# Kernel optimization log

Hardware: AMD Instinct MI355X
Metric: run time of the kernel (lower is better)

## Reference

```python
import jax, jax.numpy as jnp
import numpy as np

B, N, D = 4, 10000, 64
C, E = 2, 160000  # adj channels, edges per (graph, channel)
EPS = 1e-10


def setup_inputs() -> dict:
    key = jax.random.key(0)
    k1, k2, k3 = jax.random.split(key, 3)
    inputs = jax.random.normal(k1, (B, N, D), dtype=jnp.float32)
    edge_idx = jax.random.randint(k2, (B, C, E, 2), 0, N, dtype=jnp.int32)
    weight_a = 0.1 * jax.random.normal(k3, (C, 2 * D, 1), dtype=jnp.float32)
    return {"inputs": inputs, "edge_idx": edge_idx, "weight_a": weight_a}


def _gat_channel(x, idx, wa):
    # x: [N, D], idx: [E, 2] (col 0 = scatter/dst node, col 1 = gather/src node), wa: [2D, 1]
    n = x.shape[0]
    a1 = x[idx[:, 1]]                      # [E, D]
    a2 = x[idx[:, 0]]                      # [E, D]
    score = jnp.concatenate([a1, a2], axis=1) @ wa   # [E, 1]
    e = jnp.exp(jax.nn.leaky_relu(score, negative_slope=0.2))  # [E, 1]
    denom = jax.ops.segment_sum(e, idx[:, 0], num_segments=n)  # [N, 1]  (ii @ e)
    denom_e = denom[idx[:, 1]]             # [E, 1]  (faithful to original: gather by idx[:,1])
    alpha = e / (denom_e + EPS)            # [E, 1]
    r = jax.ops.segment_sum(alpha * a1, idx[:, 0], num_segments=n)  # [N, D]
    return jax.nn.sigmoid(r)


def _gat_graph(x, idx_all, weight_a):
    # x: [N, D], idx_all: [C, E, 2], weight_a: [C, 2D, 1]
    per_ch = jax.vmap(_gat_channel, in_axes=(None, 0, 0))(x, idx_all, weight_a)  # [C, N, D]
    return per_ch.sum(axis=0)


def reference(inputs, edge_idx, weight_a):
    # inputs: [B, N, D], edge_idx: [B, C, E, 2], weight_a: [C, 2D, 1]
    return jax.vmap(_gat_graph, in_axes=(0, 0, None))(inputs, edge_idx, weight_a)
```

## Files before the change

kernel.cpp:

```cpp
#include <hip/hip_runtime.h>

#define B_ 4
#define N_ 10000
#define D_ 64
#define C_ 2
#define E_ 160000
#define BC_ (B_ * C_)
#define SH2_ 7
#define NB2_ 128
#define G2_ 79
#define CAPF_ 2560
#define NBLK_ 125
#define EPT_ 5
#define EPB_ (256 * EPT_)
#define YBLK_ (BC_ * 40)
#define EPS_ 1e-10f

__global__ void gat_yb(const float* __restrict__ x, const float* __restrict__ wa,
                       float* __restrict__ y1, float* __restrict__ y0,
                       const int* __restrict__ eidx, int* __restrict__ gcount,
                       unsigned int* __restrict__ bpack) {
    int tid = threadIdx.x;
    if (blockIdx.x < YBLK_) {
        int bc = blockIdx.x & 7;
        int n  = (blockIdx.x >> 3) * 256 + tid;
        if (n >= N_) return;
        int b = bc / C_, c = bc % C_;
        const float4* xr = (const float4*)(x + ((size_t)b * N_ + n) * D_);
        const float4* w1 = (const float4*)(wa + (size_t)c * 2 * D_);
        const float4* w0 = w1 + D_ / 4;
        float a = 0.f, bb = 0.f;
#pragma unroll
        for (int i = 0; i < D_ / 4; ++i) {
            float4 xv = xr[i];
            float4 u = w1[i], v = w0[i];
            a  += xv.x * u.x + xv.y * u.y + xv.z * u.z + xv.w * u.w;
            bb += xv.x * v.x + xv.y * v.y + xv.z * v.z + xv.w * v.w;
        }
        y1[bc * N_ + n] = a;
        y0[bc * N_ + n] = bb;
        return;
    }
    int bid = blockIdx.x - YBLK_;
    int bc  = bid & 7;
    int blk = bid >> 3;
    const int2* ep = (const int2*)eidx + (size_t)bc * E_ + (size_t)blk * EPB_;
    __shared__ int sd[128];
    __shared__ int excl[G2_], cur[G2_], gbase[G2_];
    __shared__ unsigned int stage[EPB_];
    if (tid < 128) sd[tid] = 0;
    __syncthreads();
    unsigned int pk[EPT_];
    int gg[EPT_];
#pragma unroll
    for (int k = 0; k < EPT_; ++k) {
        int2 v = ep[k * 256 + tid];
        int g  = v.x >> SH2_;
        gg[k]  = g;
        pk[k]  = ((unsigned int)g << 21) |
                 ((unsigned int)(v.x & (NB2_ - 1)) << 14) |
                 (unsigned int)v.y;
        atomicAdd(&sd[g], 1);
    }
    __syncthreads();
    int cnt = (tid < 128) ? sd[tid] : 0;
    for (int off = 1; off < 128; off <<= 1) {
        int t = (tid < 128 && tid >= off) ? sd[tid - off] : 0;
        __syncthreads();
        if (tid < 128) sd[tid] += t;
        __syncthreads();
    }
    if (tid < G2_) {
        int ex = sd[tid] - cnt;
        excl[tid]  = ex;
        cur[tid]   = ex;
        gbase[tid] = atomicAdd(&gcount[bc * G2_ + tid], cnt);
    }
    __syncthreads();
#pragma unroll
    for (int k = 0; k < EPT_; ++k) {
        int slot = atomicAdd(&cur[gg[k]], 1);
        stage[slot] = pk[k];
    }
    __syncthreads();
#pragma unroll
    for (int k = 0; k < EPT_; ++k) {
        int idx = k * 256 + tid;
        unsigned int p = stage[idx];
        int g     = p >> 21;
        int local = idx - excl[g];
        bpack[((size_t)bc * G2_ + g) * CAPF_ + gbase[g] + local] =
            (((p >> 14) & 127u) << 16) | (p & 16383u);
    }
}

__global__ void gat_fine(const unsigned int* __restrict__ bpack,
                         const int* __restrict__ gcount,
                         const float* __restrict__ y1, const float* __restrict__ y0,
                         unsigned short* __restrict__ csr_i1,
                         int* __restrict__ rs_s, int* __restrict__ rs_e,
                         float2* __restrict__ yrd) {
    int bc = blockIdx.x & 7;
    int g  = blockIdx.x >> 3;
    int K  = gcount[bc * G2_ + g];
    int R  = (bc * G2_ + g) * CAPF_;
    const unsigned int* bp = bpack + R;
    const float* y1p = y1 + bc * N_;
    int tid = threadIdx.x;

    __shared__ int   cnt[NB2_], excl[NB2_], cur[NB2_], sd[NB2_];
    __shared__ float y0l[NB2_], den[NB2_];
    __shared__ unsigned short li1[CAPF_];

    int node = g * NB2_ + tid;
    if (tid < NB2_) {
        cnt[tid] = 0;
        den[tid] = 0.f;
        y0l[tid] = (node < N_) ? y0[bc * N_ + node] : 0.f;
    }
    __syncthreads();

    for (int j = tid; j < K; j += 256) {
        unsigned int p = bp[j];
        int ln = p >> 16;
        int i1 = p & 0xffff;
        float sc = y1p[i1] + y0l[ln];
        float ev = __expf(sc > 0.f ? sc : 0.2f * sc);
        atomicAdd(&cnt[ln], 1);
        atomicAdd(&den[ln], ev);
    }
    __syncthreads();

    int v = 0;
    if (tid < NB2_) { v = cnt[tid]; sd[tid] = v; }
    __syncthreads();
    for (int off = 1; off < NB2_; off <<= 1) {
        int t = (tid < NB2_ && tid >= off) ? sd[tid - off] : 0;
        __syncthreads();
        if (tid < NB2_) sd[tid] += t;
        __syncthreads();
    }
    if (tid < NB2_) {
        int ex = sd[tid] - v;
        excl[tid] = ex;
        cur[tid]  = ex;
        if (node < N_) {
            rs_s[bc * N_ + node] = R + ex;
            rs_e[bc * N_ + node] = R + ex + v;
            yrd[bc * N_ + node]  = make_float2(y1p[node], 1.f / (den[tid] + EPS_));
        }
    }
    __syncthreads();

    for (int j = tid; j < K; j += 256) {
        unsigned int p = bp[j];
        int slot = atomicAdd(&cur[p >> 16], 1);
        li1[slot] = (unsigned short)(p & 0xffff);
    }
    __syncthreads();

    for (int j = tid; j < K; j += 256)
        csr_i1[R + j] = li1[j];
}

__global__ void gat_acc(const float* __restrict__ x, const int* __restrict__ rs_s,
                        const int* __restrict__ rs_e,
                        const unsigned short* __restrict__ csr_i1,
                        const float2* __restrict__ yrd, const float* __restrict__ y0,
                        float* __restrict__ out) {
    int lane = threadIdx.x & 63;
    int w    = threadIdx.x >> 6;
    int b    = blockIdx.x & 3;
    int nn   = blockIdx.x >> 2;
    int n    = nn * 2 + (w >> 1);
    int c    = w & 1;
    int bc = b * C_ + c;
    const float* xb = x + (size_t)b * N_ * D_ + lane;
    const float2* yrdp = yrd + bc * N_;
    int s = rs_s[bc * N_ + n], t = rs_e[bc * N_ + n];
    float y0n = y0[bc * N_ + n];
    __shared__ float2 meta[4][64];
    float acc = 0.f;
    for (int base = s; base < t; base += 64) {
        int m = t - base; if (m > 64) m = 64;
        int a = 0; float wgt = 0.f;
        if (lane < m) {
            a = csr_i1[base + lane];
            float2 yr = yrdp[a];
            float sc = yr.x + y0n;
            wgt = __expf(sc > 0.f ? sc : 0.2f * sc) * yr.y;
        }
        meta[w][lane] = make_float2(__int_as_float(a), wgt);
        int mp = (m + 7) & ~7;
        for (int j = 0; j < mp; j += 8) {
            float2 m0 = meta[w][j],     m1 = meta[w][j + 1];
            float2 m2 = meta[w][j + 2], m3 = meta[w][j + 3];
            float2 m4 = meta[w][j + 4], m5 = meta[w][j + 5];
            float2 m6 = meta[w][j + 6], m7 = meta[w][j + 7];
            float x0 = xb[__float_as_int(m0.x) * D_], x1 = xb[__float_as_int(m1.x) * D_];
            float x2 = xb[__float_as_int(m2.x) * D_], x3 = xb[__float_as_int(m3.x) * D_];
            float x4 = xb[__float_as_int(m4.x) * D_], x5 = xb[__float_as_int(m5.x) * D_];
            float x6 = xb[__float_as_int(m6.x) * D_], x7 = xb[__float_as_int(m7.x) * D_];
            acc += m0.y * x0;
            acc += m1.y * x1;
            acc += m2.y * x2;
            acc += m3.y * x3;
            acc += m4.y * x4;
            acc += m5.y * x5;
            acc += m6.y * x6;
            acc += m7.y * x7;
        }
    }
    float sg = 1.f / (1.f + __expf(-acc));
    __shared__ float sh[2][64];
    if (c == 1) sh[w >> 1][lane] = sg;
    __syncthreads();
    if (c == 0) out[((size_t)b * N_ + n) * D_ + lane] = sg + sh[w >> 1][lane];
}

extern "C" void kernel_launch(void* const* d_in, const int* in_sizes, int n_in,
                              void* d_out, int out_size, void* d_ws, size_t ws_size,
                              hipStream_t stream) {
    const float* x    = (const float*)d_in[0];
    const int*   eidx = (const int*)d_in[1];
    const float* wa   = (const float*)d_in[2];
    float* out = (float*)d_out;

    int*    gcount = (int*)d_ws;
    float*  y1     = (float*)d_ws + 1024;
    float*  y0     = y1 + BC_ * N_;
    float2* yrd    = (float2*)(y0 + BC_ * N_);
    int*    rs_s   = (int*)(yrd + BC_ * N_);
    int*    rs_e   = rs_s + BC_ * N_;
    unsigned int* bpack = (unsigned int*)(rs_e + BC_ * N_);
    unsigned short* csr_i1 = (unsigned short*)(bpack + (size_t)BC_ * G2_ * CAPF_);

    hipMemsetAsync(gcount, 0, BC_ * G2_ * sizeof(int), stream);

    gat_yb  <<<YBLK_ + BC_ * NBLK_, 256, 0, stream>>>(x, wa, y1, y0, eidx, gcount, bpack);
    gat_fine<<<BC_ * G2_,           256, 0, stream>>>(bpack, gcount, y1, y0,
                                                      csr_i1, rs_s, rs_e, yrd);
    gat_acc <<<B_ * N_ / 2,         256, 0, stream>>>(x, rs_s, rs_e, csr_i1, yrd, y0, out);
}
```

Measured before the change: 129.3 us.

## Process four consecutive destination nodes per wavefront in gather-accumulate kernel

Each wavefront in the accumulate kernel now handles four adjacent destination nodes, whose CSR rows are contiguous. It loads their edges as one merged 64-wide chunk stream and splits the accumulation per node by row bounds. This is meant to cut the partially filled 64-lane chunks and padding work that come from short per-node edge lists (about 16 edges each), and to reduce the grid size. In exchange there is more serial per-node loop logic, fewer waves for latency hiding, and the workspace offset is shifted so the vector loads are aligned.

```diff
diff --git a/kernel.cpp b/kernel.cpp
--- a/kernel.cpp
+++ b/kernel.cpp
@@ -171,51 +171,81 @@
     int lane = threadIdx.x & 63;
     int w    = threadIdx.x >> 6;
     int b    = blockIdx.x & 3;
-    int nn   = blockIdx.x >> 2;
-    int n    = nn * 2 + (w >> 1);
+    int gp   = blockIdx.x >> 2;
     int c    = w & 1;
-    int bc = b * C_ + c;
+    int n0   = gp * 8 + (w >> 1) * 4;
+    int bc   = b * C_ + c;
     const float* xb = x + (size_t)b * N_ * D_ + lane;
     const float2* yrdp = yrd + bc * N_;
-    int s = rs_s[bc * N_ + n], t = rs_e[bc * N_ + n];
-    float y0n = y0[bc * N_ + n];
+    int4   sv  = *(const int4*)(rs_s + bc * N_ + n0);
+    int4   ev  = *(const int4*)(rs_e + bc * N_ + n0);
+    float4 y04 = *(const float4*)(y0 + bc * N_ + n0);
+    int s0 = sv.x;
+    int e0 = ev.x, e1 = ev.y, e2 = ev.z, e3 = ev.w;
     __shared__ float2 meta[4][64];
-    float acc = 0.f;
-    for (int base = s; base < t; base += 64) {
-        int m = t - base; if (m > 64) m = 64;
+    float acc0 = 0.f, acc1 = 0.f, acc2 = 0.f, acc3 = 0.f;
+    for (int base = s0; base < e3; base += 64) {
+        int idx = base + lane;
         int a = 0; float wgt = 0.f;
-        if (lane < m) {
-            a = csr_i1[base + lane];
+        if (idx < e3) {
+            a = csr_i1[idx];
             float2 yr = yrdp[a];
-            float sc = yr.x + y0n;
+            float yn = idx < e0 ? y04.x : idx < e1 ? y04.y : idx < e2 ? y04.z : y04.w;
+            float sc = yr.x + yn;
             wgt = __expf(sc > 0.f ? sc : 0.2f * sc) * yr.y;
         }
         meta[w][lane] = make_float2(__int_as_float(a), wgt);
-        int mp = (m + 7) & ~7;
-        for (int j = 0; j < mp; j += 8) {
-            float2 m0 = meta[w][j],     m1 = meta[w][j + 1];
-            float2 m2 = meta[w][j + 2], m3 = meta[w][j + 3];
-            float2 m4 = meta[w][j + 4], m5 = meta[w][j + 5];
-            float2 m6 = meta[w][j + 6], m7 = meta[w][j + 7];
-            float x0 = xb[__float_as_int(m0.x) * D_], x1 = xb[__float_as_int(m1.x) * D_];
-            float x2 = xb[__float_as_int(m2.x) * D_], x3 = xb[__float_as_int(m3.x) * D_];
-            float x4 = xb[__float_as_int(m4.x) * D_], x5 = xb[__float_as_int(m5.x) * D_];
-            float x6 = xb[__float_as_int(m6.x) * D_], x7 = xb[__float_as_int(m7.x) * D_];
-            acc += m0.y * x0;
-            acc += m1.y * x1;
-            acc += m2.y * x2;
-            acc += m3.y * x3;
-            acc += m4.y * x4;
-            acc += m5.y * x5;
-            acc += m6.y * x6;
-            acc += m7.y * x7;
-        }
-    }
-    float sg = 1.f / (1.f + __expf(-acc));
-    __shared__ float sh[2][64];
-    if (c == 1) sh[w >> 1][lane] = sg;
-    __syncthreads();
-    if (c == 0) out[((size_t)b * N_ + n) * D_ + lane] = sg + sh[w >> 1][lane];
+        int hi = (base + 64 < e3) ? base + 64 : e3;
+#define ACC_NODE(SK, EK, ACCK)                                                \
+        {                                                                     \
+            int lo = (SK > base) ? SK : base;                                 \
+            int h  = (EK < hi) ? EK : hi;                                     \
+            int j  = lo;                                                      \
+            for (; j + 4 <= h; j += 4) {                                      \
+                float2 m0 = meta[w][j - base];                                \
+                float2 m1 = meta[w][j - base + 1];                            \
+                float2 m2 = meta[w][j - base + 2];                            \
+                float2 m3 = meta[w][j - base + 3];                            \
+                float x0 = xb[__float_as_int(m0.x) * D_];                     \
+                float x1 = xb[__float_as_int(m1.x) * D_];                     \
+                float x2 = xb[__float_as_int(m2.x) * D_];                     \
+                float x3 = xb[__float_as_int(m3.x) * D_];                     \
+                ACCK += m0.y * x0;                                            \
+                ACCK += m1.y * x1;                                            \
+                ACCK += m2.y * x2;                                            \
+                ACCK += m3.y * x3;                                            \
+            }                                                                 \
+            for (; j < h; ++j) {                                              \
+                float2 mm = meta[w][j - base];                                \
+                ACCK += mm.y * xb[__float_as_int(mm.x) * D_];                 \
+            }                                                                 \
+        }
+        ACC_NODE(s0, e0, acc0)
+        ACC_NODE(e0, e1, acc1)
+        ACC_NODE(e1, e2, acc2)
+        ACC_NODE(e2, e3, acc3)
+#undef ACC_NODE
+    }
+    float4 sg;
+    sg.x = 1.f / (1.f + __expf(-acc0));
+    sg.y = 1.f / (1.f + __expf(-acc1));
+    sg.z = 1.f / (1.f + __expf(-acc2));
+    sg.w = 1.f / (1.f + __expf(-acc3));
+    __shared__ float sh[2][4][64];
+    if (c == 1) {
+        sh[w >> 1][0][lane] = sg.x;
+        sh[w >> 1][1][lane] = sg.y;
+        sh[w >> 1][2][lane] = sg.z;
+        sh[w >> 1][3][lane] = sg.w;
+    }
+    __syncthreads();
+    if (c == 0) {
+        int h = w >> 1;
+        out[((size_t)b * N_ + n0 + 0) * D_ + lane] = sg.x + sh[h][0][lane];
+        out[((size_t)b * N_ + n0 + 1) * D_ + lane] = sg.y + sh[h][1][lane];
+        out[((size_t)b * N_ + n0 + 2) * D_ + lane] = sg.z + sh[h][2][lane];
+        out[((size_t)b * N_ + n0 + 3) * D_ + lane] = sg.w + sh[h][3][lane];
+    }
 }
 
 extern "C" void kernel_launch(void* const* d_in, const int* in_sizes, int n_in,
@@ -227,7 +257,7 @@
     float* out = (float*)d_out;
 
     int*    gcount = (int*)d_ws;
-    float*  y1     = (float*)d_ws + 1024;
+    float*  y1     = (float*)d_ws + 2048;
     float*  y0     = y1 + BC_ * N_;
     float2* yrd    = (float2*)(y0 + BC_ * N_);
     int*    rs_s   = (int*)(yrd + BC_ * N_);
@@ -240,5 +270,5 @@
     gat_yb  <<<YBLK_ + BC_ * NBLK_, 256, 0, stream>>>(x, wa, y1, y0, eidx, gcount, bpack);
     gat_fine<<<BC_ * G2_,           256, 0, stream>>>(bpack, gcount, y1, y0,
                                                       csr_i1, rs_s, rs_e, yrd);
-    gat_acc <<<B_ * N_ / 2,         256, 0, stream>>>(x, rs_s, rs_e, csr_i1, yrd, y0, out);
-}
+    gat_acc <<<B_ * N_ / 8,         256, 0, stream>>>(x, rs_s, rs_e, csr_i1, yrd, y0, out);
+}
```

Result: no change. 128.6 us (-0.5%).
